# Kernel optimization log

Hardware: AMD Instinct MI355X
Metric: run time of the kernel (lower is better)

## Reference

```python
import jax, jax.numpy as jnp
import numpy as np

VAR_SCALE = 0.1


def setup_inputs() -> dict:
    key = jax.random.key(0)
    k_x, k_tc, k_task, k_in, k_out = jax.random.split(key, 5)
    B, T, IN, OUT, R = 1024, 8, 4096, 4096, 64
    x = jax.random.normal(k_x, (B, T, IN), dtype=jnp.float32)
    tensor_core = jax.random.normal(k_tc, (R, R, R), dtype=jnp.float32) * VAR_SCALE
    task_core = jax.random.normal(k_task, (T, R), dtype=jnp.float32) * VAR_SCALE
    in_core = jax.random.normal(k_in, (IN, R), dtype=jnp.float32) * VAR_SCALE
    out_core = jax.random.normal(k_out, (OUT, R), dtype=jnp.float32) * VAR_SCALE
    return {"x": x, "tensor_core": tensor_core, "task_core": task_core,
            "in_core": in_core, "out_core": out_core}


def reference(x, tensor_core, task_core, in_core, out_core):
    # Tucker weight reconstruction, faithful to the torch einsum chain.
    # W1: [T, R, R] = task_core @ tensor_core (contract first core mode)
    W = jnp.einsum('tj,jkl->tkl', task_core, tensor_core)
    # W2: [T, IN, R] = contract in_core with middle mode
    W = jnp.einsum('ij,tjk->tik', in_core, W)
    # W3: [T, IN, OUT] = contract out_core with last mode
    W = jnp.einsum('oj,tij->tio', out_core, W)
    # Batched per-task matmul: x [B, T, IN] -> y [B, T, OUT]
    y = jnp.einsum('bti,tio->bto', x, W)
    return y
```

## Files before the change

### kernel.cpp

```cpp
#include <hip/hip_runtime.h>
#include <hip/hip_bf16.h>


typedef __bf16 bf16;
typedef __bf16 bf16x8 __attribute__((ext_vector_type(8)));
typedef __bf16 bf16x4 __attribute__((ext_vector_type(4)));
typedef float  f32x4  __attribute__((ext_vector_type(4)));

__device__ __forceinline__ bf16x8 load_frag_bf16(const bf16* p) {
    return *reinterpret_cast<const bf16x8*>(p);
}

__device__ __forceinline__ bf16x8 load_frag_f32(const float* p) {
    f32x4 a = *reinterpret_cast<const f32x4*>(p);
    f32x4 b = *reinterpret_cast<const f32x4*>(p + 4);
    bf16x8 r;
    r[0] = (bf16)a[0]; r[1] = (bf16)a[1]; r[2] = (bf16)a[2]; r[3] = (bf16)a[3];
    r[4] = (bf16)b[0]; r[5] = (bf16)b[1]; r[6] = (bf16)b[2]; r[7] = (bf16)b[3];
    return r;
}

__device__ __forceinline__ f32x4 mfma16(bf16x8 a, bf16x8 b, f32x4 c) {
    return __builtin_amdgcn_mfma_f32_16x16x32_bf16(a, b, c, 0, 0, 0);
}

__global__ __launch_bounds__(256) void k_setup(
    const float* __restrict__ task,
    const float* __restrict__ tensor,
    const float* __restrict__ in_core,
    bf16* __restrict__ w1,
    bf16* __restrict__ icT)
{
    int bid = blockIdx.x;
    if (bid < 128) {
        int t    = bid >> 4;
        int idx  = (bid & 15) * 256 + threadIdx.x;
        int j    = idx >> 6;
        int k    = idx & 63;
        float acc = 0.f;
        #pragma unroll 8
        for (int m = 0; m < 64; ++m)
            acc += task[t * 64 + m] * tensor[(m * 64 + j) * 64 + k];
        w1[(t * 64 + j) * 64 + k] = (bf16)acc;
    } else {
        int idx = (bid - 128) * 256 + threadIdx.x;
        int i0  = (idx & 511) * 8;
        int j   = idx >> 9;
        bf16x8 v;
        #pragma unroll
        for (int s = 0; s < 8; ++s)
            v[s] = (bf16)in_core[(size_t)(i0 + s) * 64 + j];
        *reinterpret_cast<bf16x8*>(icT + (size_t)j * 4096 + i0) = v;
    }
}

__global__ __launch_bounds__(256) void k2_mt(
    const float* __restrict__ out_core,
    const bf16* __restrict__ w1,
    bf16* __restrict__ mt)
{
    int t    = blockIdx.x >> 6;
    int ot   = blockIdx.x & 63;
    int wave = threadIdx.x >> 6;
    int lane = threadIdx.x & 63;
    int m    = lane & 15;
    int q    = lane >> 4;
    int o0   = ot * 64 + wave * 16;

    f32x4 acc[4] = {};
    #pragma unroll
    for (int kc = 0; kc < 64; kc += 32) {
        bf16x8 a = load_frag_f32(out_core + (size_t)(o0 + m) * 64 + kc + q * 8);
        #pragma unroll
        for (int nt = 0; nt < 4; ++nt) {
            bf16x8 b = load_frag_bf16(w1 + (size_t)(t * 64 + nt * 16 + m) * 64 + kc + q * 8);
            acc[nt] = mfma16(a, b, acc[nt]);
        }
    }
    #pragma unroll
    for (int nt = 0; nt < 4; ++nt) {
        #pragma unroll
        for (int r = 0; r < 4; ++r) {
            int o = o0 + q * 4 + r;
            mt[(size_t)(t * 4096 + o) * 64 + nt * 16 + m] = (bf16)acc[nt][r];
        }
    }
}

__global__ __launch_bounds__(256) void k0_z(
    const float* __restrict__ x,
    const bf16* __restrict__ icT,
    bf16* __restrict__ z)
{
    __shared__ bf16 xs[16 * 256];
    int row_base = blockIdx.x * 16;
    int tid  = threadIdx.x;
    int r    = tid >> 4;
    int c16  = tid & 15;
    int wave = tid >> 6;
    int lane = tid & 63;
    int m    = lane & 15;
    int q    = lane >> 4;
    int n0   = wave * 16;

    const float* gsrc = x   + (size_t)(row_base + r) * 4096;
    const bf16*  bbas = icT + (size_t)(n0 + m) * 4096;

    f32x4 vA[4], vB[4];
    #pragma unroll
    for (int i = 0; i < 4; ++i)
        vA[i] = *reinterpret_cast<const f32x4*>(gsrc + c16 * 4 + i * 64);
    #pragma unroll
    for (int i = 0; i < 4; ++i)
        vB[i] = *reinterpret_cast<const f32x4*>(gsrc + 256 + c16 * 4 + i * 64);

    f32x4 acc = {};
    #pragma unroll 1
    for (int kc = 0; kc < 4096; kc += 512) {
        __syncthreads();
        #pragma unroll
        for (int i = 0; i < 4; ++i) {
            bf16x4 w;
            w[0] = (bf16)vA[i][0]; w[1] = (bf16)vA[i][1];
            w[2] = (bf16)vA[i][2]; w[3] = (bf16)vA[i][3];
            int col = c16 * 4 + i * 64;
            int u   = (col >> 3) ^ (r & 7);
            *reinterpret_cast<bf16x4*>(&xs[r * 256 + u * 8 + (col & 7)]) = w;
        }
        __syncthreads();
        if (kc + 512 < 4096) {
            #pragma unroll
            for (int i = 0; i < 4; ++i)
                vA[i] = *reinterpret_cast<const f32x4*>(gsrc + kc + 512 + c16 * 4 + i * 64);
        }
        #pragma unroll
        for (int c = 0; c < 8; ++c) {
            int u = (c * 4 + q) ^ (m & 7);
            bf16x8 a = *reinterpret_cast<const bf16x8*>(&xs[m * 256 + u * 8]);
            bf16x8 b = load_frag_bf16(bbas + kc + c * 32 + q * 8);
            acc = mfma16(a, b, acc);
        }
        __syncthreads();
        #pragma unroll
        for (int i = 0; i < 4; ++i) {
            bf16x4 w;
            w[0] = (bf16)vB[i][0]; w[1] = (bf16)vB[i][1];
            w[2] = (bf16)vB[i][2]; w[3] = (bf16)vB[i][3];
            int col = c16 * 4 + i * 64;
            int u   = (col >> 3) ^ (r & 7);
            *reinterpret_cast<bf16x4*>(&xs[r * 256 + u * 8 + (col & 7)]) = w;
        }
        __syncthreads();
        if (kc + 768 < 4096) {
            #pragma unroll
            for (int i = 0; i < 4; ++i)
                vB[i] = *reinterpret_cast<const f32x4*>(gsrc + kc + 768 + c16 * 4 + i * 64);
        }
        #pragma unroll
        for (int c = 0; c < 8; ++c) {
            int u = (c * 4 + q) ^ (m & 7);
            bf16x8 a = *reinterpret_cast<const bf16x8*>(&xs[m * 256 + u * 8]);
            bf16x8 b = load_frag_bf16(bbas + kc + 256 + c * 32 + q * 8);
            acc = mfma16(a, b, acc);
        }
    }
    bf16* dst = z + (size_t)row_base * 64;
    #pragma unroll
    for (int rr = 0; rr < 4; ++rr)
        dst[(q * 4 + rr) * 64 + n0 + m] = (bf16)acc[rr];
}

__global__ __launch_bounds__(256) void k3_y(
    const bf16* __restrict__ z,
    const bf16* __restrict__ mt,
    float* __restrict__ y)
{
    __shared__ float slab[4 * 2112];
    int bx    = blockIdx.x;
    int t     = bx >> 8;
    int rest  = bx & 255;
    int mtile = rest >> 5;
    int ntile = rest & 31;
    int wave  = threadIdx.x >> 6;
    int lane  = threadIdx.x & 63;
    int m     = lane & 15;
    int q     = lane >> 4;

    int b_base = mtile * 128 + wave * 32;
    int n_base = ntile * 128;

    f32x4 acc[2][8] = {};
    #pragma unroll
    for (int kc = 0; kc < 64; kc += 32) {
        bf16x8 a0 = load_frag_bf16(z + (size_t)((b_base + m) * 8 + t) * 64 + kc + q * 8);
        bf16x8 a1 = load_frag_bf16(z + (size_t)((b_base + 16 + m) * 8 + t) * 64 + kc + q * 8);
        #pragma unroll
        for (int nt = 0; nt < 8; ++nt) {
            bf16x8 b = load_frag_bf16(mt + (size_t)(t * 4096 + n_base + nt * 16 + m) * 64 + kc + q * 8);
            acc[0][nt] = mfma16(a0, b, acc[0][nt]);
            acc[1][nt] = mfma16(a1, b, acc[1][nt]);
        }
    }

    float* sw = slab + wave * 2112;
    #pragma unroll
    for (int sub = 0; sub < 2; ++sub) {
        #pragma unroll
        for (int nt = 0; nt < 8; ++nt) {
            #pragma unroll
            for (int r = 0; r < 4; ++r)
                sw[(q * 4 + r) * 132 + nt * 16 + m] = acc[sub][nt][r];
        }
        #pragma unroll
        for (int p = 0; p < 8; ++p) {
            int row = 2 * p + (lane >> 5);
            int cu  = lane & 31;
            f32x4 d = *reinterpret_cast<const f32x4*>(sw + row * 132 + cu * 4);
            int b   = b_base + sub * 16 + row;
            *reinterpret_cast<f32x4*>(y + (size_t)(b * 8 + t) * 4096 + n_base + cu * 4) = d;
        }
    }
}

extern "C" void kernel_launch(void* const* d_in, const int* in_sizes, int n_in,
                              void* d_out, int out_size, void* d_ws, size_t ws_size,
                              hipStream_t stream) {
    const float* x        = (const float*)d_in[0];
    const float* tensor_c = (const float*)d_in[1];
    const float* task_c   = (const float*)d_in[2];
    const float* in_c     = (const float*)d_in[3];
    const float* out_c    = (const float*)d_in[4];
    float* y = (float*)d_out;

    char* ws = (char*)d_ws;
    bf16* w1  = (bf16*)ws;
    bf16* icT = (bf16*)(ws + (64 << 10));
    bf16* mtc = (bf16*)(ws + (64 << 10) + (512 << 10));
    bf16* zb  = (bf16*)(ws + (64 << 10) + (512 << 10) + (4 << 20));

    k_setup<<<256,  256, 0, stream>>>(task_c, tensor_c, in_c, w1, icT);
    k2_mt  <<<512,  256, 0, stream>>>(out_c, w1, mtc);
    k0_z   <<<512,  256, 0, stream>>>(x, icT, zb);
    k3_y   <<<2048, 256, 0, stream>>>(zb, mtc, y);
}
```

Measured before the change: 281.2 us.

## Fuse x-projection and output-core expansion into one kernel via shared-memory z

Merges the kernel that projects x onto the rank-64 in-core basis with the kernel that expands z through the out-core/task matrix. Each block now computes a 16-row z tile for one task, keeps it in LDS, and then writes the full 4096-wide output rows for those rows. This drops the z round-trip through global memory and one launch. In exchange, each block does far more serial output work with only 512 blocks, and the 4 waves each stream a 1024-column slab of mt, so parallelism and output-write concurrency go down.

```diff
diff --git a/kernel.cpp b/kernel.cpp
--- a/kernel.cpp
+++ b/kernel.cpp
@@ -87,13 +87,18 @@
     }
 }
 
-__global__ __launch_bounds__(256) void k0_z(
+__global__ __launch_bounds__(256) void k_fused(
     const float* __restrict__ x,
     const bf16* __restrict__ icT,
-    bf16* __restrict__ z)
+    const bf16* __restrict__ mt,
+    float* __restrict__ y)
 {
-    __shared__ bf16 xs[16 * 256];
-    int row_base = blockIdx.x * 16;
+    __shared__ bf16  xs[16 * 256];
+    __shared__ bf16  zb[16 * 80];
+    __shared__ float slab[4 * 2112];
+
+    int t    = blockIdx.x & 7;
+    int b0   = (blockIdx.x >> 3) * 16;
     int tid  = threadIdx.x;
     int r    = tid >> 4;
     int c16  = tid & 15;
@@ -103,7 +108,7 @@
     int q    = lane >> 4;
     int n0   = wave * 16;
 
-    const float* gsrc = x   + (size_t)(row_base + r) * 4096;
+    const float* gsrc = x   + (size_t)((b0 + r) * 8 + t) * 4096;
     const bf16*  bbas = icT + (size_t)(n0 + m) * 4096;
 
     f32x4 vA[4], vB[4];
@@ -164,60 +169,41 @@
             acc = mfma16(a, b, acc);
         }
     }
-    bf16* dst = z + (size_t)row_base * 64;
     #pragma unroll
     for (int rr = 0; rr < 4; ++rr)
-        dst[(q * 4 + rr) * 64 + n0 + m] = (bf16)acc[rr];
-}
-
-__global__ __launch_bounds__(256) void k3_y(
-    const bf16* __restrict__ z,
-    const bf16* __restrict__ mt,
-    float* __restrict__ y)
-{
-    __shared__ float slab[4 * 2112];
-    int bx    = blockIdx.x;
-    int t     = bx >> 8;
-    int rest  = bx & 255;
-    int mtile = rest >> 5;
-    int ntile = rest & 31;
-    int wave  = threadIdx.x >> 6;
-    int lane  = threadIdx.x & 63;
-    int m     = lane & 15;
-    int q     = lane >> 4;
-
-    int b_base = mtile * 128 + wave * 32;
-    int n_base = ntile * 128;
-
-    f32x4 acc[2][8] = {};
-    #pragma unroll
-    for (int kc = 0; kc < 64; kc += 32) {
-        bf16x8 a0 = load_frag_bf16(z + (size_t)((b_base + m) * 8 + t) * 64 + kc + q * 8);
-        bf16x8 a1 = load_frag_bf16(z + (size_t)((b_base + 16 + m) * 8 + t) * 64 + kc + q * 8);
+        zb[(q * 4 + rr) * 80 + n0 + m] = (bf16)acc[rr];
+    __syncthreads();
+
+    bf16x8 a_lo = *reinterpret_cast<const bf16x8*>(zb + m * 80 + q * 8);
+    bf16x8 a_hi = *reinterpret_cast<const bf16x8*>(zb + m * 80 + 32 + q * 8);
+
+    float* sw = slab + wave * 2112;
+    const bf16* mbase = mt + ((size_t)t * 4096 + wave * 1024) * 64;
+
+    #pragma unroll 1
+    for (int g = 0; g < 8; ++g) {
+        f32x4 acc2[8] = {};
         #pragma unroll
         for (int nt = 0; nt < 8; ++nt) {
-            bf16x8 b = load_frag_bf16(mt + (size_t)(t * 4096 + n_base + nt * 16 + m) * 64 + kc + q * 8);
-            acc[0][nt] = mfma16(a0, b, acc[0][nt]);
-            acc[1][nt] = mfma16(a1, b, acc[1][nt]);
-        }
-    }
-
-    float* sw = slab + wave * 2112;
-    #pragma unroll
-    for (int sub = 0; sub < 2; ++sub) {
+            const bf16* bp = mbase + (size_t)(g * 128 + nt * 16 + m) * 64;
+            bf16x8 blo = load_frag_bf16(bp + q * 8);
+            bf16x8 bhi = load_frag_bf16(bp + 32 + q * 8);
+            acc2[nt] = mfma16(a_lo, blo, acc2[nt]);
+            acc2[nt] = mfma16(a_hi, bhi, acc2[nt]);
+        }
         #pragma unroll
         for (int nt = 0; nt < 8; ++nt) {
             #pragma unroll
-            for (int r = 0; r < 4; ++r)
-                sw[(q * 4 + r) * 132 + nt * 16 + m] = acc[sub][nt][r];
+            for (int rr = 0; rr < 4; ++rr)
+                sw[(q * 4 + rr) * 132 + nt * 16 + m] = acc2[nt][rr];
         }
         #pragma unroll
         for (int p = 0; p < 8; ++p) {
             int row = 2 * p + (lane >> 5);
             int cu  = lane & 31;
             f32x4 d = *reinterpret_cast<const f32x4*>(sw + row * 132 + cu * 4);
-            int b   = b_base + sub * 16 + row;
-            *reinterpret_cast<f32x4*>(y + (size_t)(b * 8 + t) * 4096 + n_base + cu * 4) = d;
+            *reinterpret_cast<f32x4*>(
+                y + (size_t)((b0 + row) * 8 + t) * 4096 + wave * 1024 + g * 128 + cu * 4) = d;
         }
     }
 }
@@ -236,10 +222,8 @@
     bf16* w1  = (bf16*)ws;
     bf16* icT = (bf16*)(ws + (64 << 10));
     bf16* mtc = (bf16*)(ws + (64 << 10) + (512 << 10));
-    bf16* zb  = (bf16*)(ws + (64 << 10) + (512 << 10) + (4 << 20));
-
-    k_setup<<<256,  256, 0, stream>>>(task_c, tensor_c, in_c, w1, icT);
-    k2_mt  <<<512,  256, 0, stream>>>(out_c, w1, mtc);
-    k0_z   <<<512,  256, 0, stream>>>(x, icT, zb);
-    k3_y   <<<2048, 256, 0, stream>>>(zb, mtc, y);
-}
+
+    k_setup<<<256, 256, 0, stream>>>(task_c, tensor_c, in_c, w1, icT);
+    k2_mt  <<<512, 256, 0, stream>>>(out_c, w1, mtc);
+    k_fused<<<512, 256, 0, stream>>>(x, icT, mtc, y);
+}
```

Result: no change. 283.1 us (+0.7%).
